# Optimization experiments

Measured on AMD Instinct MI355X. Metric: run time of the kernel, lower is better.

Reference implementation:

```python
import jax, jax.numpy as jnp
import numpy as np

K = 3        # kernel_size
UM = 2       # um_dim
EPS = 1e-6
SLOPE = 0.01 # F.leaky_relu default negative slope


def setup_inputs() -> dict:
    key = jax.random.key(0)
    k1, k2, k3 = jax.random.split(key, 3)
    B, C, H, Wd = 16, 64, 64, 64
    O = 64
    xx = jax.random.normal(k1, (B, C, H, Wd), dtype=jnp.float32)
    W = jax.random.normal(k2, (O, C, K, K), dtype=jnp.float32) * 0.05
    b = jax.random.normal(k3, (O,), dtype=jnp.float32) * 0.05
    return {"xx": xx, "W": W, "b": b}


def reference(xx, W, b):
    B, C, H, Wd = xx.shape
    O = W.shape[0]
    p = (K - 1) // 2
    # replicate pad (mode='replicate' in torch == 'edge' in numpy/jax)
    xp = jnp.pad(xx, ((0, 0), (0, 0), (p, p), (p, p)), mode='edge')
    # unfold -> patches[b, c, i, j, h, w] = xp[b, c, h+i, w+j]; stride==1
    pats = jnp.stack(
        [xp[:, :, i:i + H, j:j + Wd] for i in range(K) for j in range(K)],
        axis=2,
    ).reshape(B, C, K, K, H, Wd)
    # min-max "std" normalization over (channel-group, ki, kj)
    g = pats.reshape(B, C // UM, UM, K, K, H, Wd)
    stds = (g.max(axis=(1, 3, 4), keepdims=True)
            - g.min(axis=(1, 3, 4), keepdims=True))  # [B,1,UM,1,1,H,W]
    normed = (g / (stds + EPS)).reshape(B, C, K, K, H, Wd)
    # patch-conv with stride=k on the unfolded image is equivalent to this
    # per-position contraction; big[b,c,h*k+j, w*k+i] = normed[b,c,i,j,h,w]
    # so the kernel indexes as W[o, c, j, i].
    out = jnp.einsum('bcijhw,ocji->bohw', normed, W) + b[None, :, None, None]
    out = jnp.where(out >= 0, out, SLOPE * out)  # leaky_relu
    # inverse transform: re-scale by (stds + eps)
    stds_s = stds.reshape(B, 1, UM, H, Wd)
    out = out.reshape(B, O // UM, UM, H, Wd) * (stds_s + EPS)
    return out.reshape(B, O, H, Wd)
```

## Files before the change

### kernel.cpp

```cpp
#include <hip/hip_runtime.h>
#include <hip/hip_bf16.h>

#define B_  16
#define C_  64
#define H_  64
#define W_  64
#define O_  64
#define EPS 1e-6f
#define SLOPE 0.01f

typedef __bf16  bf16x8 __attribute__((ext_vector_type(8)));
typedef float   f32x4  __attribute__((ext_vector_type(4)));

#define XT_OFF   0
#define XT_SZ    36864
#define PMIN_OFF (XT_OFF + XT_SZ)
#define PMAX_OFF (PMIN_OFF + 4096)
#define SINV_OFF (PMAX_OFF + 4096)
#define SEPS_OFF (SINV_OFF + 1024)
#define SMEM_SZ  (SEPS_OFF + 1024)

__device__ __align__(16) unsigned short g_Wt[O_ * C_ * 9];

__device__ __forceinline__ unsigned short f2bf(float f) {
  unsigned u = __float_as_uint(f);
  u += 0x7fffu + ((u >> 16) & 1u);
  return (unsigned short)(u >> 16);
}

__device__ __forceinline__ int clampi(int v, int lo, int hi) {
  return v < lo ? lo : (v > hi ? hi : v);
}

__global__ void wtransform_kernel(const float* __restrict__ Wsrc) {
  int idx = blockIdx.x * 256 + threadIdx.x;
  if (idx >= O_ * C_ * 9) return;
  int i = idx % 3;
  int j = (idx / 3) % 3;
  int c = (idx / 9) % C_;
  int o = idx / (9 * C_);
  int tap = i * 3 + j;
  g_Wt[((tap * 2 + (c & 1)) * 64 + o) * 32 + (c >> 1)] = f2bf(Wsrc[idx]);
}

__launch_bounds__(512, 4)
__global__ void conv_main_kernel(const float* __restrict__ x,
                                 const float* __restrict__ bias,
                                 float* __restrict__ out) {
  __shared__ __align__(16) char smem[SMEM_SZ];
  const int tid  = threadIdx.x;
  const int lane = tid & 63;
  const int wv   = tid >> 6;

  const int bid  = (int)blockIdx.x;
  const int obid = (bid & 7) * 64 + (bid >> 3);
  const int b    = obid >> 5;
  const int h0   = (obid & 31) << 1;

  {
    const int w    = tid & 63;
    const int r    = (tid >> 6) & 3;
    const int half = tid >> 8;
    const int hr = clampi(h0 - 1 + r, 0, H_ - 1);
    const float* xb = x + ((size_t)b * C_ * H_ * W_) + hr * W_ + w;
    float mn[2] = {3.4e38f, 3.4e38f}, mx[2] = {-3.4e38f, -3.4e38f};
    #pragma unroll
    for (int pm = 0; pm < 4; ++pm) {
      const int p = pm >> 1, m = pm & 1;
      unsigned d[4];
      #pragma unroll
      for (int e = 0; e < 4; ++e) {
        const int c2a = half * 16 + m * 8 + 2 * e;
        const float f0 = xb[(2 * c2a + p) * (H_ * W_)];
        const float f1 = xb[(2 * (c2a + 1) + p) * (H_ * W_)];
        mn[p] = fminf(mn[p], fminf(f0, f1));
        mx[p] = fmaxf(mx[p], fmaxf(f0, f1));
        d[e] = (unsigned)f2bf(f0) | ((unsigned)f2bf(f1) << 16);
      }
      *(uint4*)(smem + XT_OFF + (r * 64 + w) * 144 + p * 64 + half * 32 + m * 16) =
          make_uint4(d[0], d[1], d[2], d[3]);
    }
    ((float*)(smem + PMIN_OFF))[((half * 2 + 0) * 4 + r) * 64 + w] = mn[0];
    ((float*)(smem + PMIN_OFF))[((half * 2 + 1) * 4 + r) * 64 + w] = mn[1];
    ((float*)(smem + PMAX_OFF))[((half * 2 + 0) * 4 + r) * 64 + w] = mx[0];
    ((float*)(smem + PMAX_OFF))[((half * 2 + 1) * 4 + r) * 64 + w] = mx[1];
  }

  const int l15 = lane & 15;
  const int q   = lane >> 4;
  const int hh  = wv >> 2;
  const int o0  = (wv & 3) << 4;

  bf16x8 af[9];
  #pragma unroll
  for (int t9 = 0; t9 < 9; ++t9)
    af[t9] = *(const bf16x8*)(g_Wt + ((t9 * 2 + 0) * 64 + o0 + l15) * 32 + q * 8);

  __syncthreads();

  if (tid < 256) {
    const int shh = tid >> 7, sp = (tid >> 6) & 1, sw = tid & 63;
    const float* pmin = (const float*)(smem + PMIN_OFF);
    const float* pmax = (const float*)(smem + PMAX_OFF);
    float mn = 3.4e38f, mx = -3.4e38f;
    #pragma unroll
    for (int r = 0; r < 3; ++r) {
      #pragma unroll
      for (int dw = -1; dw <= 1; ++dw) {
        const int wc = clampi(sw + dw, 0, W_ - 1);
        mn = fminf(mn, fminf(pmin[((0 * 2 + sp) * 4 + shh + r) * 64 + wc],
                             pmin[((1 * 2 + sp) * 4 + shh + r) * 64 + wc]));
        mx = fmaxf(mx, fmaxf(pmax[((0 * 2 + sp) * 4 + shh + r) * 64 + wc],
                             pmax[((1 * 2 + sp) * 4 + shh + r) * 64 + wc]));
      }
    }
    const float sv = (mx - mn) + EPS;
    ((float*)(smem + SEPS_OFF))[(shh * 2 + sp) * 64 + sw] = sv;
    ((float*)(smem + SINV_OFF))[(shh * 2 + sp) * 64 + sw] = 1.0f / sv;
  }
  __syncthreads();

  const f32x4 zero = {0.0f, 0.0f, 0.0f, 0.0f};
  f32x4 acc[2][4];
  #pragma unroll
  for (int p = 0; p < 2; ++p)
    #pragma unroll
    for (int nt = 0; nt < 4; ++nt) acc[p][nt] = zero;

  #pragma unroll
  for (int p = 0; p < 2; ++p) {
    if (p == 1) {
      #pragma unroll
      for (int t9 = 0; t9 < 9; ++t9)
        af[t9] = *(const bf16x8*)(g_Wt + ((t9 * 2 + 1) * 64 + o0 + l15) * 32 + q * 8);
    }
    #pragma unroll
    for (int ri = 0; ri < 3; ++ri) {
      const int r = hh + ri;
      #pragma unroll
      for (int nt = 0; nt < 4; ++nt) {
        bf16x8 bfr[3];
        #pragma unroll
        for (int j = 0; j < 3; ++j) {
          const int wc = clampi(nt * 16 + l15 + j - 1, 0, W_ - 1);
          bfr[j] = *(const bf16x8*)(smem + XT_OFF + (r * 64 + wc) * 144 + p * 64 + q * 16);
        }
        #pragma unroll
        for (int j = 0; j < 3; ++j)
          acc[p][nt] = __builtin_amdgcn_mfma_f32_16x16x32_bf16(
              af[ri * 3 + j], bfr[j], acc[p][nt], 0, 0, 0);
      }
    }
  }

  const float* sinv = (const float*)(smem + SINV_OFF);
  const float* seps = (const float*)(smem + SEPS_OFF);
  #pragma unroll
  for (int nt = 0; nt < 4; ++nt) {
    const int wpx = nt * 16 + l15;
    const float s0  = sinv[(hh * 2 + 0) * 64 + wpx];
    const float s1  = sinv[(hh * 2 + 1) * 64 + wpx];
    const float se0 = seps[(hh * 2 + 0) * 64 + wpx];
    const float se1 = seps[(hh * 2 + 1) * 64 + wpx];
    #pragma unroll
    for (int reg = 0; reg < 4; ++reg) {
      const int o = o0 + q * 4 + reg;
      float v = acc[0][nt][reg] * s0 + acc[1][nt][reg] * s1 + bias[o];
      v = v >= 0.0f ? v : SLOPE * v;
      v *= (o & 1) ? se1 : se0;
      out[((b * O_ + o) * H_ + (h0 + hh)) * W_ + wpx] = v;
    }
  }
}

extern "C" void kernel_launch(void* const* d_in, const int* in_sizes, int n_in,
                              void* d_out, int out_size, void* d_ws, size_t ws_size,
                              hipStream_t stream) {
  const float* x    = (const float*)d_in[0];
  const float* Wsrc = (const float*)d_in[1];
  const float* bias = (const float*)d_in[2];
  float* out = (float*)d_out;
  (void)d_ws; (void)ws_size;

  wtransform_kernel<<<144, 256, 0, stream>>>(Wsrc);
  conv_main_kernel<<<512, 512, 0, stream>>>(x, bias, out);
}
```

Measured before the change: 83.38 us.

## Enlarge row tile to four output rows per block to cut halo reloads

Each block now computes four output rows instead of two, loading a six-row halo of input into shared memory instead of four. Fewer blocks are launched, and waves are reassigned to split width tiles instead of rows. Each loaded B fragment now feeds several output-row accumulators. The aim is to cut redundant global loads of halo rows and to reuse LDS fragments. In exchange it uses more LDS and accumulator registers, lowers the occupancy bound, and launches only 256 blocks.

Result: no change. 83.33 us (-0.1%).

```diff
diff --git a/kernel.cpp b/kernel.cpp
--- a/kernel.cpp
+++ b/kernel.cpp
@@ -13,12 +13,12 @@
 typedef float   f32x4  __attribute__((ext_vector_type(4)));
 
 #define XT_OFF   0
-#define XT_SZ    36864
+#define XT_SZ    55296
 #define PMIN_OFF (XT_OFF + XT_SZ)
-#define PMAX_OFF (PMIN_OFF + 4096)
-#define SINV_OFF (PMAX_OFF + 4096)
-#define SEPS_OFF (SINV_OFF + 1024)
-#define SMEM_SZ  (SEPS_OFF + 1024)
+#define PMAX_OFF (PMIN_OFF + 6144)
+#define SINV_OFF (PMAX_OFF + 6144)
+#define SEPS_OFF (SINV_OFF + 2048)
+#define SMEM_SZ  (SEPS_OFF + 2048)
 
 __device__ __align__(16) unsigned short g_Wt[O_ * C_ * 9];
 
@@ -43,7 +43,7 @@
   g_Wt[((tap * 2 + (c & 1)) * 64 + o) * 32 + (c >> 1)] = f2bf(Wsrc[idx]);
 }
 
-__launch_bounds__(512, 4)
+__launch_bounds__(512, 2)
 __global__ void conv_main_kernel(const float* __restrict__ x,
                                  const float* __restrict__ bias,
                                  float* __restrict__ out) {
@@ -53,42 +53,49 @@
   const int wv   = tid >> 6;
 
   const int bid  = (int)blockIdx.x;
-  const int obid = (bid & 7) * 64 + (bid >> 3);
-  const int b    = obid >> 5;
-  const int h0   = (obid & 31) << 1;
+  const int obid = (bid & 7) * 32 + (bid >> 3);
+  const int b    = obid >> 4;
+  const int h0   = (obid & 15) << 2;
 
   {
     const int w    = tid & 63;
-    const int r    = (tid >> 6) & 3;
-    const int half = tid >> 8;
-    const int hr = clampi(h0 - 1 + r, 0, H_ - 1);
-    const float* xb = x + ((size_t)b * C_ * H_ * W_) + hr * W_ + w;
-    float mn[2] = {3.4e38f, 3.4e38f}, mx[2] = {-3.4e38f, -3.4e38f};
-    #pragma unroll
-    for (int pm = 0; pm < 4; ++pm) {
-      const int p = pm >> 1, m = pm & 1;
-      unsigned d[4];
-      #pragma unroll
-      for (int e = 0; e < 4; ++e) {
-        const int c2a = half * 16 + m * 8 + 2 * e;
-        const float f0 = xb[(2 * c2a + p) * (H_ * W_)];
-        const float f1 = xb[(2 * (c2a + 1) + p) * (H_ * W_)];
-        mn[p] = fminf(mn[p], fminf(f0, f1));
-        mx[p] = fmaxf(mx[p], fmaxf(f0, f1));
-        d[e] = (unsigned)f2bf(f0) | ((unsigned)f2bf(f1) << 16);
-      }
-      *(uint4*)(smem + XT_OFF + (r * 64 + w) * 144 + p * 64 + half * 32 + m * 16) =
-          make_uint4(d[0], d[1], d[2], d[3]);
-    }
-    ((float*)(smem + PMIN_OFF))[((half * 2 + 0) * 4 + r) * 64 + w] = mn[0];
-    ((float*)(smem + PMIN_OFF))[((half * 2 + 1) * 4 + r) * 64 + w] = mn[1];
-    ((float*)(smem + PMAX_OFF))[((half * 2 + 0) * 4 + r) * 64 + w] = mx[0];
-    ((float*)(smem + PMAX_OFF))[((half * 2 + 1) * 4 + r) * 64 + w] = mx[1];
+    const int slot = tid >> 6;
+    #pragma unroll
+    for (int tt = 0; tt < 2; ++tt) {
+      const int t = slot + tt * 8;
+      if (t < 12) {
+        const int r    = t % 6;
+        const int half = t / 6;
+        const int hr = clampi(h0 - 1 + r, 0, H_ - 1);
+        const float* xb = x + ((size_t)b * C_ * H_ * W_) + hr * W_ + w;
+        float mn[2] = {3.4e38f, 3.4e38f}, mx[2] = {-3.4e38f, -3.4e38f};
+        #pragma unroll
+        for (int pm = 0; pm < 4; ++pm) {
+          const int p = pm >> 1, m = pm & 1;
+          unsigned d[4];
+          #pragma unroll
+          for (int e = 0; e < 4; ++e) {
+            const int c2a = half * 16 + m * 8 + 2 * e;
+            const float f0 = xb[(2 * c2a + p) * (H_ * W_)];
+            const float f1 = xb[(2 * (c2a + 1) + p) * (H_ * W_)];
+            mn[p] = fminf(mn[p], fminf(f0, f1));
+            mx[p] = fmaxf(mx[p], fmaxf(f0, f1));
+            d[e] = (unsigned)f2bf(f0) | ((unsigned)f2bf(f1) << 16);
+          }
+          *(uint4*)(smem + XT_OFF + (r * 64 + w) * 144 + p * 64 + half * 32 + m * 16) =
+              make_uint4(d[0], d[1], d[2], d[3]);
+        }
+        ((float*)(smem + PMIN_OFF))[((half * 2 + 0) * 6 + r) * 64 + w] = mn[0];
+        ((float*)(smem + PMIN_OFF))[((half * 2 + 1) * 6 + r) * 64 + w] = mn[1];
+        ((float*)(smem + PMAX_OFF))[((half * 2 + 0) * 6 + r) * 64 + w] = mx[0];
+        ((float*)(smem + PMAX_OFF))[((half * 2 + 1) * 6 + r) * 64 + w] = mx[1];
+      }
+    }
   }
 
   const int l15 = lane & 15;
   const int q   = lane >> 4;
-  const int hh  = wv >> 2;
+  const int nth = wv >> 2;
   const int o0  = (wv & 3) << 4;
 
   bf16x8 af[9];
@@ -98,20 +105,20 @@
 
   __syncthreads();
 
-  if (tid < 256) {
+  {
     const int shh = tid >> 7, sp = (tid >> 6) & 1, sw = tid & 63;
     const float* pmin = (const float*)(smem + PMIN_OFF);
     const float* pmax = (const float*)(smem + PMAX_OFF);
     float mn = 3.4e38f, mx = -3.4e38f;
     #pragma unroll
-    for (int r = 0; r < 3; ++r) {
+    for (int rr = 0; rr < 3; ++rr) {
       #pragma unroll
       for (int dw = -1; dw <= 1; ++dw) {
         const int wc = clampi(sw + dw, 0, W_ - 1);
-        mn = fminf(mn, fminf(pmin[((0 * 2 + sp) * 4 + shh + r) * 64 + wc],
-                             pmin[((1 * 2 + sp) * 4 + shh + r) * 64 + wc]));
-        mx = fmaxf(mx, fmaxf(pmax[((0 * 2 + sp) * 4 + shh + r) * 64 + wc],
-                             pmax[((1 * 2 + sp) * 4 + shh + r) * 64 + wc]));
+        mn = fminf(mn, fminf(pmin[((0 * 2 + sp) * 6 + shh + rr) * 64 + wc],
+                             pmin[((1 * 2 + sp) * 6 + shh + rr) * 64 + wc]));
+        mx = fmaxf(mx, fmaxf(pmax[((0 * 2 + sp) * 6 + shh + rr) * 64 + wc],
+                             pmax[((1 * 2 + sp) * 6 + shh + rr) * 64 + wc]));
       }
     }
     const float sv = (mx - mn) + EPS;
@@ -121,11 +128,13 @@
   __syncthreads();
 
   const f32x4 zero = {0.0f, 0.0f, 0.0f, 0.0f};
-  f32x4 acc[2][4];
+  f32x4 acc[2][4][2];
   #pragma unroll
   for (int p = 0; p < 2; ++p)
     #pragma unroll
-    for (int nt = 0; nt < 4; ++nt) acc[p][nt] = zero;
+    for (int hh = 0; hh < 4; ++hh)
+      #pragma unroll
+      for (int n = 0; n < 2; ++n) acc[p][hh][n] = zero;
 
   #pragma unroll
   for (int p = 0; p < 2; ++p) {
@@ -135,10 +144,10 @@
         af[t9] = *(const bf16x8*)(g_Wt + ((t9 * 2 + 1) * 64 + o0 + l15) * 32 + q * 8);
     }
     #pragma unroll
-    for (int ri = 0; ri < 3; ++ri) {
-      const int r = hh + ri;
-      #pragma unroll
-      for (int nt = 0; nt < 4; ++nt) {
+    for (int r = 0; r < 6; ++r) {
+      #pragma unroll
+      for (int n = 0; n < 2; ++n) {
+        const int nt = nth * 2 + n;
         bf16x8 bfr[3];
         #pragma unroll
         for (int j = 0; j < 3; ++j) {
@@ -146,9 +155,15 @@
           bfr[j] = *(const bf16x8*)(smem + XT_OFF + (r * 64 + wc) * 144 + p * 64 + q * 16);
         }
         #pragma unroll
-        for (int j = 0; j < 3; ++j)
-          acc[p][nt] = __builtin_amdgcn_mfma_f32_16x16x32_bf16(
-              af[ri * 3 + j], bfr[j], acc[p][nt], 0, 0, 0);
+        for (int i = 0; i < 3; ++i) {
+          const int hh = r - i;
+          if (hh >= 0 && hh < 4) {
+            #pragma unroll
+            for (int j = 0; j < 3; ++j)
+              acc[p][hh][n] = __builtin_amdgcn_mfma_f32_16x16x32_bf16(
+                  af[i * 3 + j], bfr[j], acc[p][hh][n], 0, 0, 0);
+          }
+        }
       }
     }
   }
@@ -156,19 +171,23 @@
   const float* sinv = (const float*)(smem + SINV_OFF);
   const float* seps = (const float*)(smem + SEPS_OFF);
   #pragma unroll
-  for (int nt = 0; nt < 4; ++nt) {
-    const int wpx = nt * 16 + l15;
-    const float s0  = sinv[(hh * 2 + 0) * 64 + wpx];
-    const float s1  = sinv[(hh * 2 + 1) * 64 + wpx];
-    const float se0 = seps[(hh * 2 + 0) * 64 + wpx];
-    const float se1 = seps[(hh * 2 + 1) * 64 + wpx];
-    #pragma unroll
-    for (int reg = 0; reg < 4; ++reg) {
-      const int o = o0 + q * 4 + reg;
-      float v = acc[0][nt][reg] * s0 + acc[1][nt][reg] * s1 + bias[o];
-      v = v >= 0.0f ? v : SLOPE * v;
-      v *= (o & 1) ? se1 : se0;
-      out[((b * O_ + o) * H_ + (h0 + hh)) * W_ + wpx] = v;
+  for (int hh = 0; hh < 4; ++hh) {
+    #pragma unroll
+    for (int n = 0; n < 2; ++n) {
+      const int nt  = nth * 2 + n;
+      const int wpx = nt * 16 + l15;
+      const float s0  = sinv[(hh * 2 + 0) * 64 + wpx];
+      const float s1  = sinv[(hh * 2 + 1) * 64 + wpx];
+      const float se0 = seps[(hh * 2 + 0) * 64 + wpx];
+      const float se1 = seps[(hh * 2 + 1) * 64 + wpx];
+      #pragma unroll
+      for (int reg = 0; reg < 4; ++reg) {
+        const int o = o0 + q * 4 + reg;
+        float v = acc[0][hh][n][reg] * s0 + acc[1][hh][n][reg] * s1 + bias[o];
+        v = v >= 0.0f ? v : SLOPE * v;
+        v *= (o & 1) ? se1 : se0;
+        out[((b * O_ + o) * H_ + (h0 + hh)) * W_ + wpx] = v;
+      }
     }
   }
 }
@@ -183,5 +202,5 @@
   (void)d_ws; (void)ws_size;
 
   wtransform_kernel<<<144, 256, 0, stream>>>(Wsrc);
-  conv_main_kernel<<<512, 512, 0, stream>>>(x, bias, out);
-}
+  conv_main_kernel<<<256, 512, 0, stream>>>(x, bias, out);
+}
```
